# Optimization experiments

Measured on AMD Instinct MI355X. Metric: run time of the kernel, lower is better.

The kernel has to match this reference:

```python
import jax, jax.numpy as jnp
import numpy as np

B = 64          # batch
N_IN = 1_000_000  # SNPs (n_inputs)
N_OUT = 20_000    # genes (n_outputs = mask.shape[1])
KMAX = 64         # filter_size = max SNPs per gene


def setup_inputs() -> dict:
    key = jax.random.key(0)
    k1, k2, k3, k4 = jax.random.split(key, 4)
    x = jax.random.normal(k1, (B, N_IN), dtype=jnp.float32)
    kernel = jax.random.normal(k2, (KMAX, N_OUT), dtype=jnp.float32) * 0.05
    bias = jnp.zeros((N_OUT, 1), dtype=jnp.float32)
    # static COO mask encoded as padded per-gene index table + valid lengths
    gather_idx = jax.random.randint(k3, (N_OUT, KMAX), 0, N_IN, dtype=jnp.int32)
    lengths = jax.random.randint(k4, (N_OUT,), 1, KMAX + 1, dtype=jnp.int32)
    return {"x": x, "kernel": kernel, "bias": bias,
            "gather_idx": gather_idx, "lengths": lengths}


def reference(x, kernel, bias, gather_idx, lengths):
    # valid[g,k] = 1 if slot k of gene g holds a real SNP (padding mask)
    valid = (jnp.arange(KMAX, dtype=lengths.dtype)[None, :] < lengths[:, None])
    # per-gene weights, zeroed at padded slots: (G, K)
    w = jnp.where(valid, kernel.T, jnp.zeros((), dtype=kernel.dtype))
    # gather inputs per gene group: (B, G, K)
    gathered = x[:, gather_idx]
    # grouped multiply-reduce: (B, G)
    out = jnp.einsum('bgk,gk->bg', gathered, w)
    # bias per (gene, filter), filters = 1 -> output (B, G, 1)
    out = out[..., None] + bias[None, :, :]
    return out  # linear activation
```

## Files before the change

### kernel.cpp

```cpp
#include <hip/hip_runtime.h>
#include <hip/hip_bf16.h>

#define B_DIM 64
#define N_IN 1000000
#define N_OUT 20000
#define KMAX 64
#define GPB 16
#define COLS 256
#define NFULL 3906
#define TAILC 64
#define FLAG_MAGIC 1
#define FB 1250

__device__ __forceinline__ unsigned short f32_to_bf16_bits(float f) {
    __hip_bfloat16 b = __float2bfloat16(f);
    unsigned short s;
    __builtin_memcpy(&s, &b, sizeof(s));
    return s;
}
__device__ __forceinline__ unsigned int pack_bf16x2(float lo, float hi) {
    return (unsigned int)f32_to_bf16_bits(lo) | ((unsigned int)f32_to_bf16_bits(hi) << 16);
}

__global__ __launch_bounds__(256) void prep_kernel(
    const int* __restrict__ gidx, const int* __restrict__ lengths,
    unsigned char* __restrict__ flags,
    const float* __restrict__ kern, float* __restrict__ wT) {
    if (blockIdx.x < FB) {
        int tid = blockIdx.x * 256 + threadIdx.x;
        int g  = tid >> 4;
        int k4 = (tid & 15) * 4;
        int len = lengths[g];
        int4 v = *reinterpret_cast<const int4*>(&gidx[g * KMAX + k4]);
        if (k4 + 0 < len) flags[v.x] = FLAG_MAGIC;
        if (k4 + 1 < len) flags[v.y] = FLAG_MAGIC;
        if (k4 + 2 < len) flags[v.z] = FLAG_MAGIC;
        if (k4 + 3 < len) flags[v.w] = FLAG_MAGIC;
        if (tid == 0) flags[0] = FLAG_MAGIC;
        return;
    }
    __shared__ float lds[64 * 65];
    const int c0 = (blockIdx.x - FB) * 64;
    const int t  = threadIdx.x;
    const int cq = t & 63;
    const int rq = t >> 6;
#pragma unroll
    for (int i = 0; i < 16; ++i) {
        int r = i * 4 + rq;
        int c = c0 + cq;
        if (c < N_OUT) lds[r * 65 + cq] = kern[r * N_OUT + c];
    }
    __syncthreads();
#pragma unroll
    for (int i = 0; i < 16; ++i) {
        int c = i * 4 + rq;
        int r = cq;
        if (c0 + c < N_OUT) wT[(c0 + c) * 64 + r] = lds[r * 65 + c];
    }
}

__global__ __launch_bounds__(512) void transpose_x(
    const float* __restrict__ src, __hip_bfloat16* __restrict__ dst,
    const unsigned char* __restrict__ flags) {
    __shared__ unsigned int lt32[COLS * 33];
    __shared__ unsigned char f[COLS];
    const int t  = threadIdx.x;
    const bool full = blockIdx.x < NFULL;
    const size_t c0 = (size_t)blockIdx.x * COLS;
    const int CN = full ? COLS : TAILC;
    if (t < CN) f[t] = flags[c0 + t];

    if (full) {
        const int w = t >> 6;
        const int a = t & 63;
#pragma unroll
        for (int i = 0; i < 4; ++i) {
            int r0 = i * 16 + w * 2;
            float4 v0 = *reinterpret_cast<const float4*>(&src[(size_t)r0 * N_IN + c0 + a * 4]);
            float4 v1 = *reinterpret_cast<const float4*>(&src[(size_t)(r0 + 1) * N_IN + c0 + a * 4]);
            int c = a * 4, h = r0 >> 1;
            lt32[(c + 0) * 33 + h] = pack_bf16x2(v0.x, v1.x);
            lt32[(c + 1) * 33 + h] = pack_bf16x2(v0.y, v1.y);
            lt32[(c + 2) * 33 + h] = pack_bf16x2(v0.z, v1.z);
            lt32[(c + 3) * 33 + h] = pack_bf16x2(v0.w, v1.w);
        }
    } else {
        if (t < 256) {
            const int c = t & 63;
            const int rp = t >> 6;
#pragma unroll
            for (int i = 0; i < 8; ++i) {
                int r0 = i * 8 + rp * 2;
                float x0 = src[(size_t)r0 * N_IN + c0 + c];
                float x1 = src[(size_t)(r0 + 1) * N_IN + c0 + c];
                lt32[c * 33 + (r0 >> 1)] = pack_bf16x2(x0, x1);
            }
        }
    }
    __syncthreads();
    const int m  = t & 15;
    const int cb = t >> 4;
#pragma unroll
    for (int i = 0; i < 8; ++i) {
        int c = cb + 32 * i;
        if (c < CN && f[c] == FLAG_MAGIC) {
            uint2 u;
            u.x = lt32[c * 33 + 2 * m];
            u.y = lt32[c * 33 + 2 * m + 1];
            *reinterpret_cast<uint2*>(&dst[(c0 + c) * 64 + m * 4]) = u;
        }
    }
}

__global__ __launch_bounds__(1024) void gather_dot_fused(
    const __hip_bfloat16* __restrict__ xT,
    const float* __restrict__ wT,
    const int*   __restrict__ gidx,
    const int*   __restrict__ lengths,
    const float* __restrict__ bias,
    float*       __restrict__ out) {
    __shared__ float sm[64 * 17];
    const int wave = threadIdx.x >> 6;
    const int lane = threadIdx.x & 63;
    const int half = lane >> 5;
    const int l    = lane & 31;
    const int g0   = blockIdx.x * GPB;
    const int g    = g0 + wave;

    const int len = lengths[g];
    const int   idx_l = (lane < len) ? gidx[g * KMAX + lane] : 0;
    const float w_l   = (lane < len) ? wT[g * KMAX + lane] : 0.0f;

    float acc0 = 0.0f, acc1 = 0.0f;
    for (int k = 0; k < len; k += 8) {
#pragma unroll
        for (int j = 0; j < 4; ++j) {
            int   kk  = k + 2 * j + half;
            int   row = __shfl(idx_l, kk);
            float w   = __shfl(w_l, kk);
            unsigned int u = *reinterpret_cast<const unsigned int*>(
                &xT[(size_t)row * 64 + 2 * l]);
            float f0 = __uint_as_float(u << 16);
            float f1 = __uint_as_float(u & 0xFFFF0000u);
            acc0 = fmaf(f0, w, acc0);
            acc1 = fmaf(f1, w, acc1);
        }
    }
    acc0 += __shfl_xor(acc0, 32);
    acc1 += __shfl_xor(acc1, 32);
    if (half == 0) {
        sm[(2 * l + 0) * 17 + wave] = acc0;
        sm[(2 * l + 1) * 17 + wave] = acc1;
    }
    __syncthreads();
    const int b = threadIdx.x >> 4;
    const int c = threadIdx.x & 15;
    out[(size_t)b * N_OUT + g0 + c] = sm[b * 17 + c] + bias[g0 + c];
}

__global__ __launch_bounds__(256) void direct_kernel(
    const float* __restrict__ x, const float* __restrict__ kern,
    const float* __restrict__ bias, const int* __restrict__ gidx,
    const int* __restrict__ lengths, float* __restrict__ out) {
    const int wave = threadIdx.x >> 6;
    const int lane = threadIdx.x & 63;
    const int g = blockIdx.x * 4 + wave;
    if (g >= N_OUT) return;
    const int len = lengths[g];
    float acc = 0.0f;
    for (int k = 0; k < len; ++k) {
        int   idx = gidx[g * KMAX + k];
        float w   = kern[k * N_OUT + g];
        acc = fmaf(x[(size_t)lane * N_IN + idx], w, acc);
    }
    out[(size_t)lane * N_OUT + g] = acc + bias[g];
}

extern "C" void kernel_launch(void* const* d_in, const int* in_sizes, int n_in,
                              void* d_out, int out_size, void* d_ws, size_t ws_size,
                              hipStream_t stream) {
    const float* x       = (const float*)d_in[0];
    const float* kern    = (const float*)d_in[1];
    const float* bias    = (const float*)d_in[2];
    const int*   gidx    = (const int*)d_in[3];
    const int*   lengths = (const int*)d_in[4];
    float*       out     = (float*)d_out;

    const size_t xT_bytes = (size_t)N_IN * B_DIM * sizeof(__hip_bfloat16);
    const size_t wT_bytes = (size_t)N_OUT * KMAX * sizeof(float);
    const size_t fl_bytes = (size_t)N_IN;

    if (ws_size >= xT_bytes + wT_bytes + fl_bytes) {
        __hip_bfloat16* xT    = (__hip_bfloat16*)d_ws;
        float*          wT    = (float*)((char*)d_ws + xT_bytes);
        unsigned char*  flags = (unsigned char*)((char*)d_ws + xT_bytes + wT_bytes);

        prep_kernel<<<FB + (N_OUT + 63) / 64, 256, 0, stream>>>(
            gidx, lengths, flags, kern, wT);
        transpose_x<<<NFULL + 1, 512, 0, stream>>>(x, xT, flags);
        gather_dot_fused<<<N_OUT / GPB, 1024, 0, stream>>>(xT, wT, gidx, lengths, bias, out);
    } else {
        direct_kernel<<<N_OUT / 4, 256, 0, stream>>>(x, kern, bias, gidx, lengths, out);
    }
}
```

Before: 90.18 us.

## Fuse prep, transpose and gather stages into one cooperative persistent kernel

Replaces the three-kernel pipeline (flag/weight prep, x transpose to bf16, gather-dot) with a single cooperative kernel of 512 persistent blocks that separates the phases with grid-wide syncs. The intent is to remove two kernel launch gaps and tail effects between stages. The gather phase is also reworked to 8 genes per block, with each lane loading four bf16 values per row and a two-step shuffle reduction. In exchange it pays for two grid barriers and a fixed grid size that may underfill the work loops. It falls back to the old three-kernel path if the cooperative launch fails.

```diff
diff --git a/kernel.cpp b/kernel.cpp
--- a/kernel.cpp
+++ b/kernel.cpp
@@ -1,16 +1,20 @@
 #include <hip/hip_runtime.h>
 #include <hip/hip_bf16.h>
+#include <hip/hip_cooperative_groups.h>
+
+namespace cg = cooperative_groups;
 
 #define B_DIM 64
 #define N_IN 1000000
 #define N_OUT 20000
 #define KMAX 64
-#define GPB 16
 #define COLS 256
 #define NFULL 3906
 #define TAILC 64
 #define FLAG_MAGIC 1
-#define FB 1250
+#define FLAG_UNITS 625
+#define KERN_TILES 313
+#define COOP_GRID 512
 
 __device__ __forceinline__ unsigned short f32_to_bf16_bits(float f) {
     __hip_bfloat16 b = __float2bfloat16(f);
@@ -22,6 +26,142 @@
     return (unsigned int)f32_to_bf16_bits(lo) | ((unsigned int)f32_to_bf16_bits(hi) << 16);
 }
 
+__global__ __launch_bounds__(512, 4) void fused_all(
+    const float* __restrict__ x, const float* __restrict__ kern,
+    const float* __restrict__ bias, const int* __restrict__ gidx,
+    const int* __restrict__ lengths, float* __restrict__ out,
+    __hip_bfloat16* __restrict__ xT, float* __restrict__ wT,
+    unsigned char* __restrict__ flags) {
+    cg::grid_group grid = cg::this_grid();
+    __shared__ unsigned int lt32[COLS * 33];
+    __shared__ unsigned char f[COLS];
+    __shared__ float smr[64 * 9];
+    const int t  = threadIdx.x;
+    const int nb = gridDim.x;
+
+    for (int u = blockIdx.x; u < FLAG_UNITS + KERN_TILES; u += nb) {
+        if (u < FLAG_UNITS) {
+            int tid = u * 512 + t;
+            int g  = tid >> 4;
+            int k4 = (tid & 15) * 4;
+            int len = lengths[g];
+            int4 v = *reinterpret_cast<const int4*>(&gidx[g * KMAX + k4]);
+            if (k4 + 0 < len) flags[v.x] = FLAG_MAGIC;
+            if (k4 + 1 < len) flags[v.y] = FLAG_MAGIC;
+            if (k4 + 2 < len) flags[v.z] = FLAG_MAGIC;
+            if (k4 + 3 < len) flags[v.w] = FLAG_MAGIC;
+            if (tid == 0) flags[0] = FLAG_MAGIC;
+        } else {
+            float* klds = reinterpret_cast<float*>(lt32);
+            const int c0 = (u - FLAG_UNITS) * 64;
+            const int cq = t & 63;
+            const int rq = t >> 6;
+#pragma unroll
+            for (int i = 0; i < 8; ++i) {
+                int r = i * 8 + rq, c = c0 + cq;
+                if (c < N_OUT) klds[r * 65 + cq] = kern[r * N_OUT + c];
+            }
+            __syncthreads();
+#pragma unroll
+            for (int i = 0; i < 8; ++i) {
+                int c = i * 8 + rq, r = cq;
+                if (c0 + c < N_OUT) wT[(c0 + c) * 64 + r] = klds[r * 65 + c];
+            }
+        }
+    }
+    grid.sync();
+
+    for (int tile = blockIdx.x; tile <= NFULL; tile += nb) {
+        const bool full_t = tile < NFULL;
+        const size_t c0 = (size_t)tile * COLS;
+        const int CN = full_t ? COLS : TAILC;
+        if (t < CN) f[t] = flags[c0 + t];
+        if (full_t) {
+            const int w = t >> 6;
+            const int a = t & 63;
+#pragma unroll
+            for (int i = 0; i < 4; ++i) {
+                int r0 = i * 16 + w * 2;
+                float4 v0 = *reinterpret_cast<const float4*>(&x[(size_t)r0 * N_IN + c0 + a * 4]);
+                float4 v1 = *reinterpret_cast<const float4*>(&x[(size_t)(r0 + 1) * N_IN + c0 + a * 4]);
+                int c = a * 4, h = r0 >> 1;
+                lt32[(c + 0) * 33 + h] = pack_bf16x2(v0.x, v1.x);
+                lt32[(c + 1) * 33 + h] = pack_bf16x2(v0.y, v1.y);
+                lt32[(c + 2) * 33 + h] = pack_bf16x2(v0.z, v1.z);
+                lt32[(c + 3) * 33 + h] = pack_bf16x2(v0.w, v1.w);
+            }
+        } else if (t < 256) {
+            const int c = t & 63;
+            const int rp = t >> 6;
+#pragma unroll
+            for (int i = 0; i < 8; ++i) {
+                int r0 = i * 8 + rp * 2;
+                float x0 = x[(size_t)r0 * N_IN + c0 + c];
+                float x1 = x[(size_t)(r0 + 1) * N_IN + c0 + c];
+                lt32[c * 33 + (r0 >> 1)] = pack_bf16x2(x0, x1);
+            }
+        }
+        __syncthreads();
+        const int m  = t & 15;
+        const int cb = t >> 4;
+#pragma unroll
+        for (int i = 0; i < 8; ++i) {
+            int c = cb + 32 * i;
+            if (c < CN && f[c] == FLAG_MAGIC) {
+                uint2 u2;
+                u2.x = lt32[c * 33 + 2 * m];
+                u2.y = lt32[c * 33 + 2 * m + 1];
+                *reinterpret_cast<uint2*>(&xT[(c0 + c) * 64 + m * 4]) = u2;
+            }
+        }
+        __syncthreads();
+    }
+    grid.sync();
+
+    for (int u = blockIdx.x; u < N_OUT / 8; u += nb) {
+        const int wave = t >> 6;
+        const int lane = t & 63;
+        const int q = lane >> 4;
+        const int l = lane & 15;
+        const int g0 = u * 8;
+        const int g  = g0 + wave;
+        const int len = lengths[g];
+        const int   idx_l = (lane < len) ? gidx[g * KMAX + lane] : 0;
+        const float w_l   = (lane < len) ? wT[g * KMAX + lane] : 0.0f;
+
+        float a0 = 0.f, a1 = 0.f, a2 = 0.f, a3 = 0.f;
+        for (int k = 0; k < len; k += 16) {
+#pragma unroll
+            for (int j = 0; j < 4; ++j) {
+                int   kk  = k + 4 * j + q;
+                int   row = __shfl(idx_l, kk);
+                float w   = __shfl(w_l, kk);
+                uint2 uv = *reinterpret_cast<const uint2*>(&xT[(size_t)row * 64 + 4 * l]);
+                a0 = fmaf(__uint_as_float(uv.x << 16),          w, a0);
+                a1 = fmaf(__uint_as_float(uv.x & 0xFFFF0000u),  w, a1);
+                a2 = fmaf(__uint_as_float(uv.y << 16),          w, a2);
+                a3 = fmaf(__uint_as_float(uv.y & 0xFFFF0000u),  w, a3);
+            }
+        }
+        a0 += __shfl_xor(a0, 16); a0 += __shfl_xor(a0, 32);
+        a1 += __shfl_xor(a1, 16); a1 += __shfl_xor(a1, 32);
+        a2 += __shfl_xor(a2, 16); a2 += __shfl_xor(a2, 32);
+        a3 += __shfl_xor(a3, 16); a3 += __shfl_xor(a3, 32);
+        if (lane < 16) {
+            smr[(4 * l + 0) * 9 + wave] = a0;
+            smr[(4 * l + 1) * 9 + wave] = a1;
+            smr[(4 * l + 2) * 9 + wave] = a2;
+            smr[(4 * l + 3) * 9 + wave] = a3;
+        }
+        __syncthreads();
+        const int b = t >> 3, c = t & 7;
+        out[(size_t)b * N_OUT + g0 + c] = smr[b * 9 + c] + bias[g0 + c];
+        __syncthreads();
+    }
+}
+
+#define GPB 16
+#define FB 1250
 __global__ __launch_bounds__(256) void prep_kernel(
     const int* __restrict__ gidx, const int* __restrict__ lengths,
     unsigned char* __restrict__ flags,
@@ -46,15 +186,13 @@
     const int rq = t >> 6;
 #pragma unroll
     for (int i = 0; i < 16; ++i) {
-        int r = i * 4 + rq;
-        int c = c0 + cq;
+        int r = i * 4 + rq, c = c0 + cq;
         if (c < N_OUT) lds[r * 65 + cq] = kern[r * N_OUT + c];
     }
     __syncthreads();
 #pragma unroll
     for (int i = 0; i < 16; ++i) {
-        int c = i * 4 + rq;
-        int r = cq;
+        int c = i * 4 + rq, r = cq;
         if (c0 + c < N_OUT) wT[(c0 + c) * 64 + r] = lds[r * 65 + c];
     }
 }
@@ -69,7 +207,6 @@
     const size_t c0 = (size_t)blockIdx.x * COLS;
     const int CN = full ? COLS : TAILC;
     if (t < CN) f[t] = flags[c0 + t];
-
     if (full) {
         const int w = t >> 6;
         const int a = t & 63;
@@ -84,17 +221,15 @@
             lt32[(c + 2) * 33 + h] = pack_bf16x2(v0.z, v1.z);
             lt32[(c + 3) * 33 + h] = pack_bf16x2(v0.w, v1.w);
         }
-    } else {
-        if (t < 256) {
-            const int c = t & 63;
-            const int rp = t >> 6;
-#pragma unroll
-            for (int i = 0; i < 8; ++i) {
-                int r0 = i * 8 + rp * 2;
-                float x0 = src[(size_t)r0 * N_IN + c0 + c];
-                float x1 = src[(size_t)(r0 + 1) * N_IN + c0 + c];
-                lt32[c * 33 + (r0 >> 1)] = pack_bf16x2(x0, x1);
-            }
+    } else if (t < 256) {
+        const int c = t & 63;
+        const int rp = t >> 6;
+#pragma unroll
+        for (int i = 0; i < 8; ++i) {
+            int r0 = i * 8 + rp * 2;
+            float x0 = src[(size_t)r0 * N_IN + c0 + c];
+            float x1 = src[(size_t)(r0 + 1) * N_IN + c0 + c];
+            lt32[c * 33 + (r0 >> 1)] = pack_bf16x2(x0, x1);
         }
     }
     __syncthreads();
@@ -113,12 +248,9 @@
 }
 
 __global__ __launch_bounds__(1024) void gather_dot_fused(
-    const __hip_bfloat16* __restrict__ xT,
-    const float* __restrict__ wT,
-    const int*   __restrict__ gidx,
-    const int*   __restrict__ lengths,
-    const float* __restrict__ bias,
-    float*       __restrict__ out) {
+    const __hip_bfloat16* __restrict__ xT, const float* __restrict__ wT,
+    const int* __restrict__ gidx, const int* __restrict__ lengths,
+    const float* __restrict__ bias, float* __restrict__ out) {
     __shared__ float sm[64 * 17];
     const int wave = threadIdx.x >> 6;
     const int lane = threadIdx.x & 63;
@@ -126,11 +258,9 @@
     const int l    = lane & 31;
     const int g0   = blockIdx.x * GPB;
     const int g    = g0 + wave;
-
     const int len = lengths[g];
     const int   idx_l = (lane < len) ? gidx[g * KMAX + lane] : 0;
     const float w_l   = (lane < len) ? wT[g * KMAX + lane] : 0.0f;
-
     float acc0 = 0.0f, acc1 = 0.0f;
     for (int k = 0; k < len; k += 8) {
 #pragma unroll
@@ -138,12 +268,9 @@
             int   kk  = k + 2 * j + half;
             int   row = __shfl(idx_l, kk);
             float w   = __shfl(w_l, kk);
-            unsigned int u = *reinterpret_cast<const unsigned int*>(
-                &xT[(size_t)row * 64 + 2 * l]);
-            float f0 = __uint_as_float(u << 16);
-            float f1 = __uint_as_float(u & 0xFFFF0000u);
-            acc0 = fmaf(f0, w, acc0);
-            acc1 = fmaf(f1, w, acc1);
+            unsigned int u = *reinterpret_cast<const unsigned int*>(&xT[(size_t)row * 64 + 2 * l]);
+            acc0 = fmaf(__uint_as_float(u << 16), w, acc0);
+            acc1 = fmaf(__uint_as_float(u & 0xFFFF0000u), w, acc1);
         }
     }
     acc0 += __shfl_xor(acc0, 32);
@@ -195,10 +322,20 @@
         float*          wT    = (float*)((char*)d_ws + xT_bytes);
         unsigned char*  flags = (unsigned char*)((char*)d_ws + xT_bytes + wT_bytes);
 
-        prep_kernel<<<FB + (N_OUT + 63) / 64, 256, 0, stream>>>(
-            gidx, lengths, flags, kern, wT);
-        transpose_x<<<NFULL + 1, 512, 0, stream>>>(x, xT, flags);
-        gather_dot_fused<<<N_OUT / GPB, 1024, 0, stream>>>(xT, wT, gidx, lengths, bias, out);
+        void* args[] = {(void*)&x, (void*)&kern, (void*)&bias, (void*)&gidx,
+                        (void*)&lengths, (void*)&out, (void*)&xT, (void*)&wT,
+                        (void*)&flags};
+        hipError_t e = hipLaunchCooperativeKernel((const void*)fused_all,
+                                                  dim3(COOP_GRID), dim3(512),
+                                                  args, 0, stream);
+        if (e != hipSuccess) {
+            (void)hipGetLastError();
+            prep_kernel<<<FB + (N_OUT + 63) / 64, 256, 0, stream>>>(
+                gidx, lengths, flags, kern, wT);
+            transpose_x<<<NFULL + 1, 512, 0, stream>>>(x, xT, flags);
+            gather_dot_fused<<<N_OUT / GPB, 1024, 0, stream>>>(
+                xT, wT, gidx, lengths, bias, out);
+        }
     } else {
         direct_kernel<<<N_OUT / 4, 256, 0, stream>>>(x, kern, bias, gidx, lengths, out);
     }
```

After: 244.3 us. 2.71x slower.
